# Kernel optimization log

Hardware: AMD Instinct MI355X
Metric: run time of the kernel (lower is better)

The kernel has to match this reference:

```python
import jax, jax.numpy as jnp
import numpy as np

HIDDEN = 512
LATENT = 256
BATCH = 1024
SEQ_LEN = 256


def setup_inputs() -> dict:
    key = jax.random.key(0)
    ks = jax.random.split(key, 12)
    s_h = 1.0 / np.sqrt(2 * HIDDEN)
    s_c = 1.0 / np.sqrt(LATENT)
    return {
        "h": jax.random.normal(ks[0], (BATCH, HIDDEN), jnp.float32),
        "c": jax.random.normal(ks[1], (BATCH, HIDDEN), jnp.float32),
        "seq_len": SEQ_LEN,
        # init-state projections: Linear(2*hidden, latent)
        "init_h_W": jax.random.uniform(ks[2], (LATENT, 2 * HIDDEN), jnp.float32, -s_h, s_h),
        "init_h_b": jax.random.uniform(ks[3], (LATENT,), jnp.float32, -s_h, s_h),
        "init_c_W": jax.random.uniform(ks[4], (LATENT, 2 * HIDDEN), jnp.float32, -s_h, s_h),
        "init_c_b": jax.random.uniform(ks[5], (LATENT,), jnp.float32, -s_h, s_h),
        # LSTM cell: input dim = hidden, state dim = latent, gates stacked [i, f, g, o]
        "W_ih": jax.random.uniform(ks[6], (4 * LATENT, HIDDEN), jnp.float32, -s_c, s_c),
        "W_hh": jax.random.uniform(ks[7], (4 * LATENT, LATENT), jnp.float32, -s_c, s_c),
        "b_ih": jax.random.uniform(ks[8], (4 * LATENT,), jnp.float32, -s_c, s_c),
        "b_hh": jax.random.uniform(ks[9], (4 * LATENT,), jnp.float32, -s_c, s_c),
    }


def reference(h, c, seq_len, init_h_W, init_h_b, init_c_W, init_c_b, W_ih, W_hh, b_ih, b_hh):
    # init states: ELU(Linear(cat(h, c)))
    hc = jnp.concatenate([h, c], axis=1)                     # [B, 2H]
    h_t = jax.nn.elu(hc @ init_h_W.T + init_h_b)             # [B, L]
    c_t = jax.nn.elu(hc @ init_c_W.T + init_c_b)             # [B, L]

    # input to the cell is the constant encoder state h -> precompute its projection once
    x_proj = h @ W_ih.T + b_ih + b_hh                        # [B, 4L]

    def step(carry, _):
        h_t, c_t = carry
        gates = x_proj + h_t @ W_hh.T                        # [B, 4L]
        i, f, g, o = jnp.split(gates, 4, axis=1)
        c_n = jax.nn.sigmoid(f) * c_t + jax.nn.sigmoid(i) * jnp.tanh(g)
        h_n = jax.nn.sigmoid(o) * jnp.tanh(c_n)
        return (h_n, c_n), h_n

    _, ys = jax.lax.scan(step, (h_t, c_t), None, length=seq_len)  # ys: [T, B, L]
    return jnp.transpose(ys, (1, 0, 2))                      # [B, T, L]
```

## Files before the change

kernel.cpp:

```cpp
#include <hip/hip_runtime.h>
#include <stdint.h>

typedef __attribute__((ext_vector_type(4))) float f32x4;
typedef __attribute__((ext_vector_type(8))) _Float16 f16x8;

static __device__ __forceinline__ unsigned short f2h(float f) {
    union { _Float16 h; unsigned short u; } v;
    v.h = (_Float16)f;
    return v.u;
}
static __device__ __forceinline__ f16x8 as_f16x8(uint4 v) {
    union { uint4 u; f16x8 s; } x; x.u = v; return x.s;
}
static __device__ __forceinline__ float sigmoid_fast(float x) {
    return __builtin_amdgcn_rcpf(1.0f + __builtin_amdgcn_exp2f(-1.4426950408889634f * x));
}
static __device__ __forceinline__ float tanh_fast(float x) {
    return 1.0f - 2.0f * __builtin_amdgcn_rcpf(1.0f + __builtin_amdgcn_exp2f(2.8853900817779268f * x));
}
static __device__ __forceinline__ void lds_barrier() {
    __builtin_amdgcn_s_waitcnt(0xc07f);
    __builtin_amdgcn_s_barrier();
}

__global__ __launch_bounds__(256) void convert_all(
    const float* __restrict__ h, const float* __restrict__ c,
    const float* __restrict__ iWh, const float* __restrict__ iWc,
    const float* __restrict__ Wih, const float* __restrict__ Whh,
    unsigned short* __restrict__ hc_h, unsigned short* __restrict__ iWh_h,
    unsigned short* __restrict__ iWc_h, unsigned short* __restrict__ Wih_h,
    unsigned short* __restrict__ Whh_h) {
    int i = blockIdx.x * 256 + threadIdx.x;
    const float* src; unsigned short* dst;
    if (i < 131072) {
        int base = i * 4, r = base >> 9, cc = base & 511;
        src = h + base; dst = hc_h + r * 1024 + cc;
    } else if (i < 262144) {
        int j = i - 131072; int base = j * 4, r = base >> 9, cc = base & 511;
        src = c + base; dst = hc_h + r * 1024 + 512 + cc;
    } else if (i < 327680) { int j = i - 262144; src = iWh + j * 4; dst = iWh_h + j * 4; }
    else if (i < 393216)   { int j = i - 327680; src = iWc + j * 4; dst = iWc_h + j * 4; }
    else if (i < 524288)   { int j = i - 393216; src = Wih + j * 4; dst = Wih_h + j * 4; }
    else                   { int j = i - 524288; src = Whh + j * 4; dst = Whh_h + j * 4; }
    float4 v = *(const float4*)src;
    dst[0] = f2h(v.x); dst[1] = f2h(v.y); dst[2] = f2h(v.z); dst[3] = f2h(v.w);
}

__global__ __launch_bounds__(256) void gemm_bt(
    const unsigned short* __restrict__ A, const unsigned short* __restrict__ W,
    float* __restrict__ C, const float* __restrict__ b1, const float* __restrict__ b2,
    int K, int lda, int N, int do_elu) {
    __shared__ unsigned short As[64][40];
    __shared__ unsigned short Bs[64][40];
    int tid = threadIdx.x;
    int lane = tid & 63, wv = tid >> 6;
    int q = lane >> 4, l15 = lane & 15;
    int Mbase = blockIdx.x * 64, Nbase = blockIdx.y * 64;
    int ldrow = tid >> 2, seg = tid & 3;
    const unsigned short* Ap = A + (size_t)(Mbase + ldrow) * lda + seg * 8;
    const unsigned short* Wp = W + (size_t)(Nbase + ldrow) * K + seg * 8;
    f32x4 acc[4] = {};
    for (int k0 = 0; k0 < K; k0 += 32) {
        uint4 av = *(const uint4*)(Ap + k0);
        uint4 wvv = *(const uint4*)(Wp + k0);
        __syncthreads();
        *(uint4*)(&As[ldrow][seg * 8]) = av;
        *(uint4*)(&Bs[ldrow][seg * 8]) = wvv;
        __syncthreads();
        f16x8 af = *(const f16x8*)(&As[wv * 16 + l15][q * 8]);
#pragma unroll
        for (int nt = 0; nt < 4; nt++) {
            f16x8 bf = *(const f16x8*)(&Bs[nt * 16 + l15][q * 8]);
            acc[nt] = __builtin_amdgcn_mfma_f32_16x16x32_f16(af, bf, acc[nt], 0, 0, 0);
        }
    }
#pragma unroll
    for (int nt = 0; nt < 4; nt++) {
        int col = Nbase + nt * 16 + l15;
        float bias = b1[col] + (b2 ? b2[col] : 0.0f);
#pragma unroll
        for (int r = 0; r < 4; r++) {
            int row = Mbase + wv * 16 + q * 4 + r;
            float v = acc[nt][r] + bias;
            if (do_elu) v = v > 0.0f ? v : (__builtin_amdgcn_exp2f(1.4426950408889634f * v) - 1.0f);
            C[(size_t)row * N + col] = v;
        }
    }
}

__global__ __launch_bounds__(256) void gemm_init(
    const unsigned short* __restrict__ A,
    const unsigned short* __restrict__ W0, const unsigned short* __restrict__ W1,
    float* __restrict__ C0, float* __restrict__ C1,
    const float* __restrict__ bias0, const float* __restrict__ bias1) {
    const unsigned short* W = blockIdx.z ? W1 : W0;
    float* C = blockIdx.z ? C1 : C0;
    const float* bias = blockIdx.z ? bias1 : bias0;
    __shared__ unsigned short As[64][40];
    __shared__ unsigned short Bs[64][40];
    int tid = threadIdx.x;
    int lane = tid & 63, wv = tid >> 6;
    int q = lane >> 4, l15 = lane & 15;
    int Mbase = blockIdx.x * 64, Nbase = blockIdx.y * 64;
    int ldrow = tid >> 2, seg = tid & 3;
    const unsigned short* Ap = A + (size_t)(Mbase + ldrow) * 1024 + seg * 8;
    const unsigned short* Wp = W + (size_t)(Nbase + ldrow) * 1024 + seg * 8;
    f32x4 acc[4] = {};
    for (int k0 = 0; k0 < 1024; k0 += 32) {
        uint4 av = *(const uint4*)(Ap + k0);
        uint4 wvv = *(const uint4*)(Wp + k0);
        __syncthreads();
        *(uint4*)(&As[ldrow][seg * 8]) = av;
        *(uint4*)(&Bs[ldrow][seg * 8]) = wvv;
        __syncthreads();
        f16x8 af = *(const f16x8*)(&As[wv * 16 + l15][q * 8]);
#pragma unroll
        for (int nt = 0; nt < 4; nt++) {
            f16x8 bf = *(const f16x8*)(&Bs[nt * 16 + l15][q * 8]);
            acc[nt] = __builtin_amdgcn_mfma_f32_16x16x32_f16(af, bf, acc[nt], 0, 0, 0);
        }
    }
#pragma unroll
    for (int nt = 0; nt < 4; nt++) {
        int col = Nbase + nt * 16 + l15;
        float b = bias[col];
#pragma unroll
        for (int r = 0; r < 4; r++) {
            int row = Mbase + wv * 16 + q * 4 + r;
            float v = acc[nt][r] + b;
            v = v > 0.0f ? v : (__builtin_amdgcn_exp2f(1.4426950408889634f * v) - 1.0f);
            C[(size_t)row * 256 + col] = v;
        }
    }
}

#define HB_STRIDE 264
#define HB_HALF   (16 * HB_STRIDE)
#define WLDS_OFF  (2 * HB_HALF * 2)
#define LSTM_LDS_BYTES (WLDS_OFF + 16 * 8 * 64 * 16)

__global__ __launch_bounds__(1024, 4) void lstm_rec(
    const unsigned short* __restrict__ Whh,
    const float* __restrict__ xp,
    const float* __restrict__ h0,
    const float* __restrict__ c0,
    const int* __restrict__ seq_len,
    float* __restrict__ out)
{
    extern __shared__ unsigned char smem[];
    unsigned short* hbuf = (unsigned short*)smem;
    unsigned char* wlds = smem + WLDS_OFF;
    int tid = threadIdx.x;
    int lane = tid & 63, wv = tid >> 6;
    int q = lane >> 4, l15 = lane & 15;
    int T = *seq_len;
    int rowbase = blockIdx.x * 16;

    const unsigned short* wbase = Whh + ((wv << 4) + l15) * 256 + q * 8;

    uint4 wreg[8];
#pragma unroll
    for (int kt = 0; kt < 2; kt++)
#pragma unroll
        for (int g = 0; g < 4; g++)
            wreg[kt * 4 + g] = *(const uint4*)(wbase + (size_t)g * 65536 + kt * 32);
#pragma unroll
    for (int kt = 2; kt < 4; kt++)
#pragma unroll
        for (int g = 0; g < 4; g++) {
            uint4 v = *(const uint4*)(wbase + (size_t)g * 65536 + kt * 32);
            *(uint4*)(wlds + ((size_t)((wv * 8) + (kt - 2) * 4 + g) * 64 + lane) * 16) = v;
        }

    float xpr[16];
#pragma unroll
    for (int g = 0; g < 4; g++)
#pragma unroll
        for (int r = 0; r < 4; r++)
            xpr[g * 4 + r] = xp[(size_t)(rowbase + q * 4 + r) * 1024 + g * 256 + wv * 16 + l15];

    float creg[4];
#pragma unroll
    for (int r = 0; r < 4; r++)
        creg[r] = c0[(size_t)(rowbase + q * 4 + r) * 256 + wv * 16 + l15];

    {
        int e = tid * 4;
        int r = e >> 8, cc = e & 255;
        float4 v = *(const float4*)(h0 + (size_t)(rowbase + r) * 256 + cc);
        unsigned short* d = hbuf + r * HB_STRIDE + cc;
        d[0] = f2h(v.x); d[1] = f2h(v.y); d[2] = f2h(v.z); d[3] = f2h(v.w);
    }
    __syncthreads();

    uint4 sbuf[4];
#pragma unroll
    for (int g = 0; g < 4; g++) sbuf[g] = *(const uint4*)(wbase + (size_t)g * 65536 + 4 * 32);

    for (int t = 0; t < T; t++) {
        unsigned short* hc = hbuf + (t & 1) * HB_HALF;
        f32x4 acc[4];
#pragma unroll
        for (int g = 0; g < 4; g++) {
            acc[g][0] = xpr[g * 4 + 0]; acc[g][1] = xpr[g * 4 + 1];
            acc[g][2] = xpr[g * 4 + 2]; acc[g][3] = xpr[g * 4 + 3];
        }
#pragma unroll
        for (int kt = 0; kt < 2; kt++) {
            f16x8 af = *(const f16x8*)(hc + l15 * HB_STRIDE + kt * 32 + q * 8);
#pragma unroll
            for (int g = 0; g < 4; g++)
                acc[g] = __builtin_amdgcn_mfma_f32_16x16x32_f16(af, as_f16x8(wreg[kt * 4 + g]), acc[g], 0, 0, 0);
        }
#pragma unroll
        for (int kt = 2; kt < 4; kt++) {
            f16x8 af = *(const f16x8*)(hc + l15 * HB_STRIDE + kt * 32 + q * 8);
#pragma unroll
            for (int g = 0; g < 4; g++) {
                f16x8 bf = *(const f16x8*)(wlds + ((size_t)((wv * 8) + (kt - 2) * 4 + g) * 64 + lane) * 16);
                acc[g] = __builtin_amdgcn_mfma_f32_16x16x32_f16(af, bf, acc[g], 0, 0, 0);
            }
        }
#pragma unroll
        for (int kt = 4; kt < 8; kt++) {
            f16x8 af = *(const f16x8*)(hc + l15 * HB_STRIDE + kt * 32 + q * 8);
            int nkt = (kt < 7) ? (kt + 1) : 4;
#pragma unroll
            for (int g = 0; g < 4; g++) {
                acc[g] = __builtin_amdgcn_mfma_f32_16x16x32_f16(af, as_f16x8(sbuf[g]), acc[g], 0, 0, 0);
                sbuf[g] = *(const uint4*)(wbase + (size_t)g * 65536 + nkt * 32);
            }
        }
        unsigned short* hn = hbuf + ((t + 1) & 1) * HB_HALF;
#pragma unroll
        for (int r = 0; r < 4; r++) {
            float ig = sigmoid_fast(acc[0][r]);
            float fg = sigmoid_fast(acc[1][r]);
            float gg = tanh_fast(acc[2][r]);
            float og = sigmoid_fast(acc[3][r]);
            float cn = fg * creg[r] + ig * gg;
            creg[r] = cn;
            float hv = og * tanh_fast(cn);
            out[((size_t)(rowbase + q * 4 + r) * T + t) * 256 + wv * 16 + l15] = hv;
            hn[(q * 4 + r) * HB_STRIDE + wv * 16 + l15] = f2h(hv);
        }
        lds_barrier();
    }
}

extern "C" void kernel_launch(void* const* d_in, const int* in_sizes, int n_in,
                              void* d_out, int out_size, void* d_ws, size_t ws_size,
                              hipStream_t stream) {
    const float* h   = (const float*)d_in[0];
    const float* c   = (const float*)d_in[1];
    const int*   seqp= (const int*)d_in[2];
    const float* iWh = (const float*)d_in[3];
    const float* ibh = (const float*)d_in[4];
    const float* iWc = (const float*)d_in[5];
    const float* ibc = (const float*)d_in[6];
    const float* Wih = (const float*)d_in[7];
    const float* Whh = (const float*)d_in[8];
    const float* bih = (const float*)d_in[9];
    const float* bhh = (const float*)d_in[10];
    float* out = (float*)d_out;
    unsigned char* ws = (unsigned char*)d_ws;

    unsigned short* hc_h  = (unsigned short*)(ws + 0);
    unsigned short* iWh_h = (unsigned short*)(ws + 2097152);
    unsigned short* iWc_h = (unsigned short*)(ws + 2621440);
    unsigned short* Wih_h = (unsigned short*)(ws + 3145728);
    unsigned short* Whh_h = (unsigned short*)(ws + 4194304);
    float* h0 = (float*)(ws + 4718592);
    float* c0 = (float*)(ws + 5767168);
    float* xp = (float*)(ws + 6815744);

    hipFuncSetAttribute(reinterpret_cast<const void*>(lstm_rec),
                        hipFuncAttributeMaxDynamicSharedMemorySize, LSTM_LDS_BYTES);

    convert_all<<<2304, 256, 0, stream>>>(h, c, iWh, iWc, Wih, Whh,
                                          hc_h, iWh_h, iWc_h, Wih_h, Whh_h);

    gemm_init<<<dim3(16, 4, 2), 256, 0, stream>>>(hc_h, iWh_h, iWc_h, h0, c0, ibh, ibc);
    gemm_bt<<<dim3(16, 16), 256, 0, stream>>>(hc_h, Wih_h, xp, bih, bhh, 512, 1024, 1024, 0);

    lstm_rec<<<64, 1024, LSTM_LDS_BYTES, stream>>>(Whh_h, xp, h0, c0, seqp, out);
}
```

Baseline: 1.355 ms.

## Double-buffer streamed Whh tiles and reverse k-order for half the waves

The recurrent loop is split into forward and reverse k-tile orderings. Waves 0-7 start with register and LDS tiles, while waves 8-15 start with the tiles streamed from global memory, so the waves stagger their LDS and global traffic. The streamed weight tiles are now double-buffered, giving each global load two k-steps to land. Register pinning via empty asm, waves_per_eu(4,4), and precomputed output pointers try to keep weights and inputs resident in VGPRs and cut address arithmetic, at the cost of more register pressure and possible spills.

```diff
diff --git a/kernel.cpp b/kernel.cpp
--- a/kernel.cpp
+++ b/kernel.cpp
@@ -9,9 +9,6 @@
     v.h = (_Float16)f;
     return v.u;
 }
-static __device__ __forceinline__ f16x8 as_f16x8(uint4 v) {
-    union { uint4 u; f16x8 s; } x; x.u = v; return x.s;
-}
 static __device__ __forceinline__ float sigmoid_fast(float x) {
     return __builtin_amdgcn_rcpf(1.0f + __builtin_amdgcn_exp2f(-1.4426950408889634f * x));
 }
@@ -22,6 +19,7 @@
     __builtin_amdgcn_s_waitcnt(0xc07f);
     __builtin_amdgcn_s_barrier();
 }
+#define PIN(x) asm volatile("" : "+v"(x))
 
 __global__ __launch_bounds__(256) void convert_all(
     const float* __restrict__ h, const float* __restrict__ c,
@@ -139,7 +137,86 @@
 #define WLDS_OFF  (2 * HB_HALF * 2)
 #define LSTM_LDS_BYTES (WLDS_OFF + 16 * 8 * 64 * 16)
 
-__global__ __launch_bounds__(1024, 4) void lstm_rec(
+template<bool FWD>
+static __device__ __forceinline__ void rec_loop(
+    int T, unsigned short* __restrict__ hbuf, const unsigned char* __restrict__ wlds,
+    const unsigned short* __restrict__ wbase,
+    f16x8 (&wreg)[8], float (&xpr)[16], float (&creg)[4],
+    float* __restrict__ out, int rowbase, int lane, int wv, int q, int l15)
+{
+    constexpr int seq0 = FWD ? 4 : 7, seq1 = FWD ? 5 : 6, seq2 = FWD ? 6 : 5, seq3 = FWD ? 7 : 4;
+    f16x8 sbuf[2][4];
+#pragma unroll
+    for (int g = 0; g < 4; g++) {
+        sbuf[0][g] = *(const f16x8*)(wbase + (size_t)g * 65536 + seq0 * 32);
+        sbuf[1][g] = *(const f16x8*)(wbase + (size_t)g * 65536 + seq1 * 32);
+    }
+    float* outp[4];
+#pragma unroll
+    for (int r = 0; r < 4; r++)
+        outp[r] = out + (size_t)(rowbase + q * 4 + r) * T * 256 + wv * 16 + l15;
+
+    const unsigned short* hA0 = hbuf + l15 * HB_STRIDE + q * 8;
+
+    for (int t = 0; t < T; t++) {
+        const unsigned short* hc = hA0 + (t & 1) * HB_HALF;
+        f32x4 acc[4];
+#pragma unroll
+        for (int g = 0; g < 4; g++) {
+            acc[g][0] = xpr[g * 4 + 0]; acc[g][1] = xpr[g * 4 + 1];
+            acc[g][2] = xpr[g * 4 + 2]; acc[g][3] = xpr[g * 4 + 3];
+        }
+
+#define REG_KT(kt) { \
+            f16x8 af = *(const f16x8*)(hc + (kt) * 32); \
+            _Pragma("unroll") for (int g = 0; g < 4; g++) \
+                acc[g] = __builtin_amdgcn_mfma_f32_16x16x32_f16(af, wreg[(kt) * 4 + g], acc[g], 0, 0, 0); }
+#define LDS_KT(kt) { \
+            f16x8 af = *(const f16x8*)(hc + (kt) * 32); \
+            _Pragma("unroll") for (int g = 0; g < 4; g++) { \
+                f16x8 bf = *(const f16x8*)(wlds + ((size_t)((wv * 8) + ((kt) - 2) * 4 + g) * 64 + lane) * 16); \
+                acc[g] = __builtin_amdgcn_mfma_f32_16x16x32_f16(af, bf, acc[g], 0, 0, 0); } }
+#define STR_KT(i, kt, nkt) { \
+            f16x8 af = *(const f16x8*)(hc + (kt) * 32); \
+            _Pragma("unroll") for (int g = 0; g < 4; g++) { \
+                acc[g] = __builtin_amdgcn_mfma_f32_16x16x32_f16(af, sbuf[(i) & 1][g], acc[g], 0, 0, 0); \
+                sbuf[(i) & 1][g] = *(const f16x8*)(wbase + (size_t)g * 65536 + (nkt) * 32); } }
+
+        if (FWD) {
+            REG_KT(0) REG_KT(1)
+            LDS_KT(2) LDS_KT(3)
+            STR_KT(0, seq0, seq2) STR_KT(1, seq1, seq3)
+            STR_KT(2, seq2, seq0) STR_KT(3, seq3, seq1)
+        } else {
+            STR_KT(0, seq0, seq2) STR_KT(1, seq1, seq3)
+            STR_KT(2, seq2, seq0) STR_KT(3, seq3, seq1)
+            LDS_KT(3) LDS_KT(2)
+            REG_KT(1) REG_KT(0)
+        }
+#undef REG_KT
+#undef LDS_KT
+#undef STR_KT
+
+        unsigned short* hn = hbuf + ((t + 1) & 1) * HB_HALF;
+#pragma unroll
+        for (int r = 0; r < 4; r++) {
+            float ig = sigmoid_fast(acc[0][r]);
+            float fg = sigmoid_fast(acc[1][r]);
+            float gg = tanh_fast(acc[2][r]);
+            float og = sigmoid_fast(acc[3][r]);
+            float cn = fg * creg[r] + ig * gg;
+            creg[r] = cn;
+            float hv = og * tanh_fast(cn);
+            outp[r][0] = hv;
+            outp[r] += 256;
+            hn[(q * 4 + r) * HB_STRIDE + wv * 16 + l15] = f2h(hv);
+        }
+        lds_barrier();
+    }
+}
+
+__global__ __launch_bounds__(1024, 4) __attribute__((amdgpu_waves_per_eu(4, 4)))
+void lstm_rec(
     const unsigned short* __restrict__ Whh,
     const float* __restrict__ xp,
     const float* __restrict__ h0,
@@ -158,12 +235,15 @@
 
     const unsigned short* wbase = Whh + ((wv << 4) + l15) * 256 + q * 8;
 
-    uint4 wreg[8];
+    f16x8 wreg[8];
 #pragma unroll
     for (int kt = 0; kt < 2; kt++)
 #pragma unroll
         for (int g = 0; g < 4; g++)
-            wreg[kt * 4 + g] = *(const uint4*)(wbase + (size_t)g * 65536 + kt * 32);
+            wreg[kt * 4 + g] = *(const f16x8*)(wbase + (size_t)g * 65536 + kt * 32);
+    PIN(wreg[0]); PIN(wreg[1]); PIN(wreg[2]); PIN(wreg[3]);
+    PIN(wreg[4]); PIN(wreg[5]); PIN(wreg[6]); PIN(wreg[7]);
+
 #pragma unroll
     for (int kt = 2; kt < 4; kt++)
 #pragma unroll
@@ -178,6 +258,8 @@
 #pragma unroll
         for (int r = 0; r < 4; r++)
             xpr[g * 4 + r] = xp[(size_t)(rowbase + q * 4 + r) * 1024 + g * 256 + wv * 16 + l15];
+#pragma unroll
+    for (int i = 0; i < 16; i++) PIN(xpr[i]);
 
     float creg[4];
 #pragma unroll
@@ -193,59 +275,10 @@
     }
     __syncthreads();
 
-    uint4 sbuf[4];
-#pragma unroll
-    for (int g = 0; g < 4; g++) sbuf[g] = *(const uint4*)(wbase + (size_t)g * 65536 + 4 * 32);
-
-    for (int t = 0; t < T; t++) {
-        unsigned short* hc = hbuf + (t & 1) * HB_HALF;
-        f32x4 acc[4];
-#pragma unroll
-        for (int g = 0; g < 4; g++) {
-            acc[g][0] = xpr[g * 4 + 0]; acc[g][1] = xpr[g * 4 + 1];
-            acc[g][2] = xpr[g * 4 + 2]; acc[g][3] = xpr[g * 4 + 3];
-        }
-#pragma unroll
-        for (int kt = 0; kt < 2; kt++) {
-            f16x8 af = *(const f16x8*)(hc + l15 * HB_STRIDE + kt * 32 + q * 8);
-#pragma unroll
-            for (int g = 0; g < 4; g++)
-                acc[g] = __builtin_amdgcn_mfma_f32_16x16x32_f16(af, as_f16x8(wreg[kt * 4 + g]), acc[g], 0, 0, 0);
-        }
-#pragma unroll
-        for (int kt = 2; kt < 4; kt++) {
-            f16x8 af = *(const f16x8*)(hc + l15 * HB_STRIDE + kt * 32 + q * 8);
-#pragma unroll
-            for (int g = 0; g < 4; g++) {
-                f16x8 bf = *(const f16x8*)(wlds + ((size_t)((wv * 8) + (kt - 2) * 4 + g) * 64 + lane) * 16);
-                acc[g] = __builtin_amdgcn_mfma_f32_16x16x32_f16(af, bf, acc[g], 0, 0, 0);
-            }
-        }
-#pragma unroll
-        for (int kt = 4; kt < 8; kt++) {
-            f16x8 af = *(const f16x8*)(hc + l15 * HB_STRIDE + kt * 32 + q * 8);
-            int nkt = (kt < 7) ? (kt + 1) : 4;
-#pragma unroll
-            for (int g = 0; g < 4; g++) {
-                acc[g] = __builtin_amdgcn_mfma_f32_16x16x32_f16(af, as_f16x8(sbuf[g]), acc[g], 0, 0, 0);
-                sbuf[g] = *(const uint4*)(wbase + (size_t)g * 65536 + nkt * 32);
-            }
-        }
-        unsigned short* hn = hbuf + ((t + 1) & 1) * HB_HALF;
-#pragma unroll
-        for (int r = 0; r < 4; r++) {
-            float ig = sigmoid_fast(acc[0][r]);
-            float fg = sigmoid_fast(acc[1][r]);
-            float gg = tanh_fast(acc[2][r]);
-            float og = sigmoid_fast(acc[3][r]);
-            float cn = fg * creg[r] + ig * gg;
-            creg[r] = cn;
-            float hv = og * tanh_fast(cn);
-            out[((size_t)(rowbase + q * 4 + r) * T + t) * 256 + wv * 16 + l15] = hv;
-            hn[(q * 4 + r) * HB_STRIDE + wv * 16 + l15] = f2h(hv);
-        }
-        lds_barrier();
-    }
+    if (wv < 8)
+        rec_loop<true >(T, hbuf, wlds, wbase, wreg, xpr, creg, out, rowbase, lane, wv, q, l15);
+    else
+        rec_loop<false>(T, hbuf, wlds, wbase, wreg, xpr, creg, out, rowbase, lane, wv, q, l15);
 }
 
 extern "C" void kernel_launch(void* const* d_in, const int* in_sizes, int n_in,
```

After: 1.504 ms. 1.11x slower.
